# Performance work log

Measured on AMD Instinct MI355X. Metric: run time of the kernel, lower is better.

The kernel has to match this reference:

```python
import jax, jax.numpy as jnp
import numpy as np

N_NODES = 50000
N_EDGES = 800000
IN_FEAT = 128
H_FEAT = 64
NUM_HEADS = 4
NEG_SLOPE = 0.2  # DGL GATConv default LeakyReLU slope


def _gat_conv(feat, src, dst, W, attn_l, attn_r, bias, num_heads, out_feats):
    # feat: [N, Din]; W: [Din, H*F]; attn_l/attn_r: [H, F]; bias: [H*F]
    N = feat.shape[0]
    h = (feat @ W).reshape(N, num_heads, out_feats)          # [N, H, F]
    el = jnp.sum(h * attn_l, axis=-1)                        # [N, H]
    er = jnp.sum(h * attn_r, axis=-1)                        # [N, H]
    e = jax.nn.leaky_relu(el[src] + er[dst], NEG_SLOPE)      # [E, H]
    # segment softmax over incoming edges of each destination node
    m = jax.ops.segment_max(e, dst, num_segments=N)          # [N, H]
    ex = jnp.exp(e - m[dst])                                 # [E, H]
    s = jax.ops.segment_sum(ex, dst, num_segments=N)         # [N, H]
    alpha = ex / s[dst]                                      # [E, H]
    # attn_drop omitted (eval-mode deterministic reference)
    msg = h[src] * alpha[:, :, None]                         # [E, H, F]
    out = jax.ops.segment_sum(msg, dst, num_segments=N)      # [N, H, F]
    return out + bias.reshape(1, num_heads, out_feats)


def setup_inputs() -> dict:
    key = jax.random.key(0)
    ks = jax.random.split(key, 16)
    feat = jax.random.normal(ks[0], (N_NODES, IN_FEAT), dtype=jnp.float32)
    src = jax.random.randint(ks[1], (N_EDGES,), 0, N_NODES)
    dst = jax.random.randint(ks[2], (N_EDGES,), 0, N_NODES)
    sc = 0.1
    H, F = NUM_HEADS, H_FEAT
    params = {
        'W1': jax.random.normal(ks[3], (IN_FEAT, H * F), dtype=jnp.float32) * sc,
        'al1': jax.random.normal(ks[4], (H, F), dtype=jnp.float32) * sc,
        'ar1': jax.random.normal(ks[5], (H, F), dtype=jnp.float32) * sc,
        'b1': jnp.zeros((H * F,), dtype=jnp.float32),
        'W2': jax.random.normal(ks[6], (H * F, H * F), dtype=jnp.float32) * sc,
        'al2': jax.random.normal(ks[7], (H, F), dtype=jnp.float32) * sc,
        'ar2': jax.random.normal(ks[8], (H, F), dtype=jnp.float32) * sc,
        'b2': jnp.zeros((H * F,), dtype=jnp.float32),
        'W3': jax.random.normal(ks[9], (H * F, F), dtype=jnp.float32) * sc,
        'al3': jax.random.normal(ks[10], (1, F), dtype=jnp.float32) * sc,
        'ar3': jax.random.normal(ks[11], (1, F), dtype=jnp.float32) * sc,
        'b3': jnp.zeros((F,), dtype=jnp.float32),
    }
    return {'feat': feat, 'src': src, 'dst': dst, **params}


def reference(feat, src, dst, W1, al1, ar1, b1, W2, al2, ar2, b2, W3, al3, ar3, b3):
    h = _gat_conv(feat, src, dst, W1, al1, ar1, b1, NUM_HEADS, H_FEAT)
    h = jax.nn.relu(h.reshape(h.shape[0], -1))               # flatten(1) + relu
    h = _gat_conv(h, src, dst, W2, al2, ar2, b2, NUM_HEADS, H_FEAT)
    h = jax.nn.relu(h.reshape(h.shape[0], -1))
    h = _gat_conv(h, src, dst, W3, al3, ar3, b3, 1, H_FEAT)
    return h.mean(axis=1)                                    # [N, h_feat]
```

## Files before the change

### kernel.cpp

```cpp
#include <hip/hip_runtime.h>
#include <math.h>

#define N_NODES 50000
#define N_EDGES 800000

typedef short bf8 __attribute__((ext_vector_type(8)));
typedef float f4x __attribute__((ext_vector_type(4)));
typedef float f2v __attribute__((ext_vector_type(2)));
typedef unsigned short us8 __attribute__((ext_vector_type(8)));

__device__ __forceinline__ unsigned short f2bf(float x) {
  unsigned u = __float_as_uint(x);
  unsigned r = (u + 0x7fff + ((u >> 16) & 1)) >> 16;
  return (unsigned short)r;
}
__device__ __forceinline__ float bf2f(unsigned short b) {
  return __uint_as_float(((unsigned)b) << 16);
}
__device__ __forceinline__ unsigned pack2(float lo, float hi) {
  return (unsigned)f2bf(lo) | ((unsigned)f2bf(hi) << 16);
}
__device__ __forceinline__ f2v bfpair(unsigned d) {
  f2v r;
  r.x = __uint_as_float(d << 16);
  r.y = __uint_as_float(d & 0xffff0000u);
  return r;
}

template <int ABF16>
__global__ __launch_bounds__(256) void gemm_mfma_k(
    const void* __restrict__ Xv, const float* __restrict__ W,
    unsigned short* __restrict__ Yb, float* __restrict__ el,
    float* __restrict__ er, const float* __restrict__ al,
    const float* __restrict__ ar, int N, int K, int M) {
  __shared__ unsigned short As[128][40];
  __shared__ unsigned short Bs[64][40];
  const int tile_n = blockIdx.x * 128;
  const int cb = blockIdx.y * 64;
  const int t = threadIdx.x;
  const int wave = t >> 6, lane = t & 63;
  const int quad = lane >> 4, l16 = lane & 15;

  f4x acc[2][4];
#pragma unroll
  for (int i = 0; i < 2; ++i)
#pragma unroll
    for (int j = 0; j < 4; ++j) acc[i][j] = (f4x){0.f, 0.f, 0.f, 0.f};

  const int ar_ = t >> 1;
  const int ac0 = (t & 1) * 16;
  const int bn = t & 63;
  const int bkq = t >> 6;

  for (int k0 = 0; k0 < K; k0 += 32) {
    if (ABF16) {
      const unsigned short* Xb = (const unsigned short*)Xv;
      int gr = tile_n + ar_;
      us8 u0 = (us8)0, u1 = (us8)0;
      if (gr < N) {
        const unsigned short* s = Xb + (size_t)gr * K + k0 + ac0;
        u0 = *(const us8*)(s + 0);
        u1 = *(const us8*)(s + 8);
      }
      *(us8*)&As[ar_][ac0] = u0;
      *(us8*)&As[ar_][ac0 + 8] = u1;
    } else {
      const float* X = (const float*)Xv;
      int gr = tile_n + ar_;
      uint4 u0, u1;
      if (gr < N) {
        const float* s = X + (size_t)gr * K + k0 + ac0;
        float4 a = *(const float4*)(s + 0);
        float4 b = *(const float4*)(s + 4);
        float4 c = *(const float4*)(s + 8);
        float4 d = *(const float4*)(s + 12);
        u0 = make_uint4(pack2(a.x, a.y), pack2(a.z, a.w),
                        pack2(b.x, b.y), pack2(b.z, b.w));
        u1 = make_uint4(pack2(c.x, c.y), pack2(c.z, c.w),
                        pack2(d.x, d.y), pack2(d.z, d.w));
      } else {
        u0 = make_uint4(0, 0, 0, 0);
        u1 = make_uint4(0, 0, 0, 0);
      }
      *(uint4*)&As[ar_][ac0] = u0;
      *(uint4*)&As[ar_][ac0 + 8] = u1;
    }
    {
      const float* s = W + (size_t)(k0 + bkq * 8) * M + cb + bn;
      float w0 = s[0 * M], w1 = s[1 * M], w2 = s[2 * M], w3 = s[3 * M];
      float w4 = s[4 * M], w5 = s[5 * M], w6 = s[6 * M], w7 = s[7 * M];
      uint4 u = make_uint4(pack2(w0, w1), pack2(w2, w3), pack2(w4, w5),
                           pack2(w6, w7));
      *(uint4*)&Bs[bn][bkq * 8] = u;
    }
    __syncthreads();
    bf8 afrag[2], bfrag[4];
#pragma unroll
    for (int rt = 0; rt < 2; ++rt)
      afrag[rt] = *(const bf8*)&As[wave * 32 + rt * 16 + l16][quad * 8];
#pragma unroll
    for (int ct = 0; ct < 4; ++ct)
      bfrag[ct] = *(const bf8*)&Bs[ct * 16 + l16][quad * 8];
#pragma unroll
    for (int rt = 0; rt < 2; ++rt)
#pragma unroll
      for (int ct = 0; ct < 4; ++ct)
        acc[rt][ct] = __builtin_amdgcn_mfma_f32_16x16x32_bf16(
            afrag[rt], bfrag[ct], acc[rt][ct], 0, 0, 0);
    __syncthreads();
  }
  const int H = M >> 6;
  const int head = cb >> 6;
  float al4[4], ar4[4];
#pragma unroll
  for (int ct = 0; ct < 4; ++ct) {
    al4[ct] = al[cb + ct * 16 + l16];
    ar4[ct] = ar[cb + ct * 16 + l16];
  }
#pragma unroll
  for (int rt = 0; rt < 2; ++rt) {
#pragma unroll
    for (int r = 0; r < 4; ++r) {
      int row = tile_n + wave * 32 + rt * 16 + quad * 4 + r;
      float pl = 0.f, pr = 0.f;
#pragma unroll
      for (int ct = 0; ct < 4; ++ct) {
        float y = acc[rt][ct][r];
        pl += y * al4[ct];
        pr += y * ar4[ct];
        if (row < N) Yb[(size_t)row * M + cb + ct * 16 + l16] = f2bf(y);
      }
#pragma unroll
      for (int off = 1; off < 16; off <<= 1) {
        pl += __shfl_xor(pl, off);
        pr += __shfl_xor(pr, off);
      }
      if (l16 == 0 && row < N) {
        el[row * H + head] = pl;
        er[row * H + head] = pr;
      }
    }
  }
}

__global__ __launch_bounds__(256) void count_deg_k(
    const int* __restrict__ dst, int* __restrict__ deg, int E) {
  int e = blockIdx.x * blockDim.x + threadIdx.x;
  if (e < E) atomicAdd(&deg[dst[e]], 1);
}

__global__ __launch_bounds__(256) void alloc_rows_k(
    const int* __restrict__ deg, int* __restrict__ rowstart,
    int* __restrict__ cursor, int* __restrict__ gcounter, int N) {
  int i = blockIdx.x * blockDim.x + threadIdx.x;
  int lane = threadIdx.x & 63;
  int d = (i < N) ? deg[i] : 0;
  int x = d;
#pragma unroll
  for (int off = 1; off < 64; off <<= 1) {
    int t = __shfl_up(x, off);
    if (lane >= off) x += t;
  }
  int wsum = __shfl(x, 63);
  int base = 0;
  if (lane == 63) base = atomicAdd(gcounter, wsum);
  base = __shfl(base, 63);
  if (i < N) {
    int mystart = base + x - d;
    rowstart[i] = mystart;
    cursor[i] = mystart;
  }
}

__global__ __launch_bounds__(256) void scatter_k(
    const int* __restrict__ src, const int* __restrict__ dst,
    int* __restrict__ cursor, int* __restrict__ src_sorted, int E) {
  int e = blockIdx.x * blockDim.x + threadIdx.x;
  if (e < E) {
    int p = atomicAdd(&cursor[dst[e]], 1);
    src_sorted[p] = src[e];
  }
}

template <int RELU>
__global__ __launch_bounds__(256) void node_agg4_k(
    const unsigned short* __restrict__ hb, const float* __restrict__ el,
    const float* __restrict__ er, const int* __restrict__ rowstart,
    const int* __restrict__ rowend, const int* __restrict__ src_sorted,
    float* __restrict__ albuf, const float* __restrict__ bias,
    unsigned short* __restrict__ outb, int N) {
  int node = blockIdx.x * 4 + (threadIdx.x >> 6);
  int lane = threadIdx.x & 63;
  if (node >= N) return;
  int start = rowstart[node], end = rowend[node];
  int head1 = lane & 3;
  int slot = lane >> 2;
  float er_v = er[node * 4 + head1];
  float ssum = 0.f;
  for (int p = start + slot; p < end; p += 16) {
    int s = src_sorted[p];
    float v = el[s * 4 + head1] + er_v;
    v = (v >= 0.f) ? v : 0.2f * v;
    float ex = __expf(v);
    ssum += ex;
    albuf[p * 4 + head1] = ex;
  }
#pragma unroll
  for (int off = 4; off < 64; off <<= 1) ssum += __shfl_xor(ssum, off);
  float inv_s = (end > start) ? 1.f / ssum : 0.f;
  int eslot = lane >> 5;
  int flane = lane & 31;
  int fo8 = flane << 3;
  int headf = fo8 >> 6;
  float inv_f = __shfl(inv_s, headf);
  __builtin_amdgcn_s_waitcnt(0);
  f2v acc2[4];
#pragma unroll
  for (int q = 0; q < 4; ++q) acc2[q] = (f2v){0.f, 0.f};
  if (end > start) {
    int src_first = src_sorted[start];
    for (int p0 = start; p0 < end; p0 += 16) {
      int sj[8];
      float aj[8];
#pragma unroll
      for (int j = 0; j < 8; ++j) {
        int p = p0 + 2 * j + eslot;
        bool v = p < end;
        sj[j] = v ? src_sorted[p] : src_first;
        aj[j] = v ? albuf[p * 4 + headf] : 0.f;
      }
#pragma unroll
      for (int j = 0; j < 8; ++j) {
        uint4 d = *(const uint4*)(hb + (size_t)sj[j] * 256 + fo8);
        f2v a2 = (f2v){aj[j], aj[j]};
        acc2[0] += bfpair(d.x) * a2;
        acc2[1] += bfpair(d.y) * a2;
        acc2[2] += bfpair(d.z) * a2;
        acc2[3] += bfpair(d.w) * a2;
      }
    }
  }
  float acc[8];
#pragma unroll
  for (int q = 0; q < 4; ++q) {
    acc[2 * q] = acc2[q].x;
    acc[2 * q + 1] = acc2[q].y;
  }
#pragma unroll
  for (int q = 0; q < 8; ++q) acc[q] += __shfl_xor(acc[q], 32);
  if (eslot == 0) {
    us8 o;
#pragma unroll
    for (int q = 0; q < 8; ++q) {
      float v = acc[q] * inv_f + bias[fo8 + q];
      if (RELU) v = fmaxf(v, 0.f);
      o[q] = f2bf(v);
    }
    *(us8*)(outb + (size_t)node * 256 + fo8) = o;
  }
}

__global__ __launch_bounds__(256) void node_agg1_k(
    const unsigned short* __restrict__ hb, const float* __restrict__ el,
    const float* __restrict__ er, const int* __restrict__ rowstart,
    const int* __restrict__ rowend, const int* __restrict__ src_sorted,
    float* __restrict__ albuf, const float* __restrict__ bias,
    float* __restrict__ out, int N) {
  int node = blockIdx.x * 4 + (threadIdx.x >> 6);
  int lane = threadIdx.x & 63;
  if (node >= N) return;
  int start = rowstart[node], end = rowend[node];
  float er_v = er[node];
  float ssum = 0.f;
  for (int p = start + lane; p < end; p += 64) {
    float v = el[src_sorted[p]] + er_v;
    v = (v >= 0.f) ? v : 0.2f * v;
    float ex = __expf(v);
    ssum += ex;
    albuf[p] = ex;
  }
#pragma unroll
  for (int off = 1; off < 64; off <<= 1) ssum += __shfl_xor(ssum, off);
  float inv_s = (end > start) ? 1.f / ssum : 0.f;
  int eslot = lane >> 3;
  int flane = lane & 7;
  int fo8 = flane << 3;
  __builtin_amdgcn_s_waitcnt(0);
  f2v acc2[4];
#pragma unroll
  for (int q = 0; q < 4; ++q) acc2[q] = (f2v){0.f, 0.f};
  if (end > start) {
    int src_first = src_sorted[start];
    for (int p0 = start; p0 < end; p0 += 32) {
      int sj[4];
      float aj[4];
#pragma unroll
      for (int j = 0; j < 4; ++j) {
        int p = p0 + 8 * j + eslot;
        bool v = p < end;
        sj[j] = v ? src_sorted[p] : src_first;
        aj[j] = v ? albuf[p] : 0.f;
      }
#pragma unroll
      for (int j = 0; j < 4; ++j) {
        uint4 d = *(const uint4*)(hb + (size_t)sj[j] * 64 + fo8);
        f2v a2 = (f2v){aj[j], aj[j]};
        acc2[0] += bfpair(d.x) * a2;
        acc2[1] += bfpair(d.y) * a2;
        acc2[2] += bfpair(d.z) * a2;
        acc2[3] += bfpair(d.w) * a2;
      }
    }
  }
  float acc[8];
#pragma unroll
  for (int q = 0; q < 4; ++q) {
    acc[2 * q] = acc2[q].x;
    acc[2 * q + 1] = acc2[q].y;
  }
#pragma unroll
  for (int off = 8; off < 64; off <<= 1)
#pragma unroll
    for (int q = 0; q < 8; ++q) acc[q] += __shfl_xor(acc[q], off);
  if (eslot == 0) {
    float* o = out + (size_t)node * 64 + fo8;
#pragma unroll
    for (int q = 0; q < 8; ++q) o[q] = acc[q] * inv_s + bias[fo8 + q];
  }
}

extern "C" void kernel_launch(void* const* d_in, const int* in_sizes, int n_in,
                              void* d_out, int out_size, void* d_ws,
                              size_t ws_size, hipStream_t stream) {
  const float* feat = (const float*)d_in[0];
  const int* src = (const int*)d_in[1];
  const int* dst = (const int*)d_in[2];
  const float* W1 = (const float*)d_in[3];
  const float* al1 = (const float*)d_in[4];
  const float* ar1 = (const float*)d_in[5];
  const float* b1 = (const float*)d_in[6];
  const float* W2 = (const float*)d_in[7];
  const float* al2 = (const float*)d_in[8];
  const float* ar2 = (const float*)d_in[9];
  const float* b2 = (const float*)d_in[10];
  const float* W3 = (const float*)d_in[11];
  const float* al3 = (const float*)d_in[12];
  const float* ar3 = (const float*)d_in[13];
  const float* b3 = (const float*)d_in[14];
  float* out = (float*)d_out;

  unsigned short* hb = (unsigned short*)d_ws;
  unsigned short* fb = hb + (size_t)N_NODES * 256;
  float* el = (float*)(fb + (size_t)N_NODES * 256);
  float* er = el + (size_t)N_NODES * 4;
  int* rowstart = (int*)(er + (size_t)N_NODES * 4);
  int* cursor = rowstart + N_NODES;
  int* deg = cursor + N_NODES;
  int* gcounter = deg + N_NODES;
  int* src_sorted = gcounter + 1;
  float* albuf = (float*)(src_sorted + N_EDGES);

  const int N = N_NODES, E = N_EDGES;
  const int GX = (N + 127) / 128;

  hipMemsetAsync(deg, 0, (size_t)(N + 1) * sizeof(int), stream);
  hipLaunchKernelGGL(count_deg_k, dim3((E + 255) / 256), dim3(256), 0, stream,
                     dst, deg, E);
  hipLaunchKernelGGL(alloc_rows_k, dim3((N + 255) / 256), dim3(256), 0, stream,
                     deg, rowstart, cursor, gcounter, N);
  hipLaunchKernelGGL(scatter_k, dim3((E + 255) / 256), dim3(256), 0, stream,
                     src, dst, cursor, src_sorted, E);

  hipLaunchKernelGGL((gemm_mfma_k<0>), dim3(GX, 4), dim3(256), 0, stream, feat,
                     W1, hb, el, er, al1, ar1, N, 128, 256);
  hipLaunchKernelGGL((node_agg4_k<1>), dim3((N + 3) / 4), dim3(256), 0, stream,
                     hb, el, er, rowstart, cursor, src_sorted, albuf, b1, fb,
                     N);

  hipLaunchKernelGGL((gemm_mfma_k<1>), dim3(GX, 4), dim3(256), 0, stream, fb,
                     W2, hb, el, er, al2, ar2, N, 256, 256);
  hipLaunchKernelGGL((node_agg4_k<1>), dim3((N + 3) / 4), dim3(256), 0, stream,
                     hb, el, er, rowstart, cursor, src_sorted, albuf, b2, fb,
                     N);

  hipLaunchKernelGGL((gemm_mfma_k<1>), dim3(GX, 1), dim3(256), 0, stream, fb,
                     W3, hb, el, er, al3, ar3, N, 256, 64);
  hipLaunchKernelGGL(node_agg1_k, dim3((N + 3) / 4), dim3(256), 0, stream, hb,
                     el, er, rowstart, cursor, src_sorted, albuf, b3, out, N);
}
```

Before: 425.7 us.

## Double-buffer GEMM LDS tiles, vectorize CSR build, shrink aggregation edge batches

The GEMM now keeps two LDS buffers and prefetches the next K tile into registers while MFMAs run on the current one, which removes one barrier per iteration. Degree counting and scatter each handle two edges per thread through int2 loads. The aggregation kernels process half as many edges per loop iteration, which lowers register pressure but exposes less memory-level parallelism per wave.

```diff
diff --git a/kernel.cpp b/kernel.cpp
--- a/kernel.cpp
+++ b/kernel.cpp
@@ -33,8 +33,8 @@
     unsigned short* __restrict__ Yb, float* __restrict__ el,
     float* __restrict__ er, const float* __restrict__ al,
     const float* __restrict__ ar, int N, int K, int M) {
-  __shared__ unsigned short As[128][40];
-  __shared__ unsigned short Bs[64][40];
+  __shared__ unsigned short As[2][128][40];
+  __shared__ unsigned short Bs[2][64][40];
   const int tile_n = blockIdx.x * 128;
   const int cb = blockIdx.y * 64;
   const int t = threadIdx.x;
@@ -51,63 +51,66 @@
   const int ac0 = (t & 1) * 16;
   const int bn = t & 63;
   const int bkq = t >> 6;
-
-  for (int k0 = 0; k0 < K; k0 += 32) {
+  const int gr = tile_n + ar_;
+
+  uint4 a_u0, a_u1, b_u;
+  auto load_tile = [&](int k0) {
     if (ABF16) {
       const unsigned short* Xb = (const unsigned short*)Xv;
-      int gr = tile_n + ar_;
       us8 u0 = (us8)0, u1 = (us8)0;
       if (gr < N) {
         const unsigned short* s = Xb + (size_t)gr * K + k0 + ac0;
         u0 = *(const us8*)(s + 0);
         u1 = *(const us8*)(s + 8);
       }
-      *(us8*)&As[ar_][ac0] = u0;
-      *(us8*)&As[ar_][ac0 + 8] = u1;
+      a_u0 = *(const uint4*)&u0;
+      a_u1 = *(const uint4*)&u1;
     } else {
       const float* X = (const float*)Xv;
-      int gr = tile_n + ar_;
-      uint4 u0, u1;
       if (gr < N) {
         const float* s = X + (size_t)gr * K + k0 + ac0;
         float4 a = *(const float4*)(s + 0);
         float4 b = *(const float4*)(s + 4);
         float4 c = *(const float4*)(s + 8);
         float4 d = *(const float4*)(s + 12);
-        u0 = make_uint4(pack2(a.x, a.y), pack2(a.z, a.w),
-                        pack2(b.x, b.y), pack2(b.z, b.w));
-        u1 = make_uint4(pack2(c.x, c.y), pack2(c.z, c.w),
-                        pack2(d.x, d.y), pack2(d.z, d.w));
+        a_u0 = make_uint4(pack2(a.x, a.y), pack2(a.z, a.w),
+                          pack2(b.x, b.y), pack2(b.z, b.w));
+        a_u1 = make_uint4(pack2(c.x, c.y), pack2(c.z, c.w),
+                          pack2(d.x, d.y), pack2(d.z, d.w));
       } else {
-        u0 = make_uint4(0, 0, 0, 0);
-        u1 = make_uint4(0, 0, 0, 0);
-      }
-      *(uint4*)&As[ar_][ac0] = u0;
-      *(uint4*)&As[ar_][ac0 + 8] = u1;
+        a_u0 = make_uint4(0, 0, 0, 0);
+        a_u1 = make_uint4(0, 0, 0, 0);
+      }
     }
-    {
-      const float* s = W + (size_t)(k0 + bkq * 8) * M + cb + bn;
-      float w0 = s[0 * M], w1 = s[1 * M], w2 = s[2 * M], w3 = s[3 * M];
-      float w4 = s[4 * M], w5 = s[5 * M], w6 = s[6 * M], w7 = s[7 * M];
-      uint4 u = make_uint4(pack2(w0, w1), pack2(w2, w3), pack2(w4, w5),
-                           pack2(w6, w7));
-      *(uint4*)&Bs[bn][bkq * 8] = u;
-    }
+    const float* s = W + (size_t)(k0 + bkq * 8) * M + cb + bn;
+    float w0 = s[0 * M], w1 = s[1 * M], w2 = s[2 * M], w3 = s[3 * M];
+    float w4 = s[4 * M], w5 = s[5 * M], w6 = s[6 * M], w7 = s[7 * M];
+    b_u = make_uint4(pack2(w0, w1), pack2(w2, w3), pack2(w4, w5),
+                     pack2(w6, w7));
+  };
+
+  load_tile(0);
+  int cur = 0;
+  for (int k0 = 0; k0 < K; k0 += 32) {
+    *(uint4*)&As[cur][ar_][ac0] = a_u0;
+    *(uint4*)&As[cur][ar_][ac0 + 8] = a_u1;
+    *(uint4*)&Bs[cur][bn][bkq * 8] = b_u;
     __syncthreads();
+    if (k0 + 32 < K) load_tile(k0 + 32);
     bf8 afrag[2], bfrag[4];
 #pragma unroll
     for (int rt = 0; rt < 2; ++rt)
-      afrag[rt] = *(const bf8*)&As[wave * 32 + rt * 16 + l16][quad * 8];
+      afrag[rt] = *(const bf8*)&As[cur][wave * 32 + rt * 16 + l16][quad * 8];
 #pragma unroll
     for (int ct = 0; ct < 4; ++ct)
-      bfrag[ct] = *(const bf8*)&Bs[ct * 16 + l16][quad * 8];
+      bfrag[ct] = *(const bf8*)&Bs[cur][ct * 16 + l16][quad * 8];
 #pragma unroll
     for (int rt = 0; rt < 2; ++rt)
 #pragma unroll
       for (int ct = 0; ct < 4; ++ct)
         acc[rt][ct] = __builtin_amdgcn_mfma_f32_16x16x32_bf16(
             afrag[rt], bfrag[ct], acc[rt][ct], 0, 0, 0);
-    __syncthreads();
+    cur ^= 1;
   }
   const int H = M >> 6;
   const int head = cb >> 6;
@@ -144,9 +147,13 @@
 }
 
 __global__ __launch_bounds__(256) void count_deg_k(
-    const int* __restrict__ dst, int* __restrict__ deg, int E) {
-  int e = blockIdx.x * blockDim.x + threadIdx.x;
-  if (e < E) atomicAdd(&deg[dst[e]], 1);
+    const int2* __restrict__ dst2, int* __restrict__ deg, int E2) {
+  int i = blockIdx.x * blockDim.x + threadIdx.x;
+  if (i < E2) {
+    int2 d = dst2[i];
+    atomicAdd(&deg[d.x], 1);
+    atomicAdd(&deg[d.y], 1);
+  }
 }
 
 __global__ __launch_bounds__(256) void alloc_rows_k(
@@ -173,12 +180,16 @@
 }
 
 __global__ __launch_bounds__(256) void scatter_k(
-    const int* __restrict__ src, const int* __restrict__ dst,
-    int* __restrict__ cursor, int* __restrict__ src_sorted, int E) {
-  int e = blockIdx.x * blockDim.x + threadIdx.x;
-  if (e < E) {
-    int p = atomicAdd(&cursor[dst[e]], 1);
-    src_sorted[p] = src[e];
+    const int2* __restrict__ src2, const int2* __restrict__ dst2,
+    int* __restrict__ cursor, int* __restrict__ src_sorted, int E2) {
+  int i = blockIdx.x * blockDim.x + threadIdx.x;
+  if (i < E2) {
+    int2 s = src2[i];
+    int2 d = dst2[i];
+    int p0 = atomicAdd(&cursor[d.x], 1);
+    src_sorted[p0] = s.x;
+    int p1 = atomicAdd(&cursor[d.y], 1);
+    src_sorted[p1] = s.y;
   }
 }
 
@@ -219,18 +230,18 @@
   for (int q = 0; q < 4; ++q) acc2[q] = (f2v){0.f, 0.f};
   if (end > start) {
     int src_first = src_sorted[start];
-    for (int p0 = start; p0 < end; p0 += 16) {
-      int sj[8];
-      float aj[8];
-#pragma unroll
-      for (int j = 0; j < 8; ++j) {
+    for (int p0 = start; p0 < end; p0 += 8) {
+      int sj[4];
+      float aj[4];
+#pragma unroll
+      for (int j = 0; j < 4; ++j) {
         int p = p0 + 2 * j + eslot;
         bool v = p < end;
         sj[j] = v ? src_sorted[p] : src_first;
         aj[j] = v ? albuf[p * 4 + headf] : 0.f;
       }
 #pragma unroll
-      for (int j = 0; j < 8; ++j) {
+      for (int j = 0; j < 4; ++j) {
         uint4 d = *(const uint4*)(hb + (size_t)sj[j] * 256 + fo8);
         f2v a2 = (f2v){aj[j], aj[j]};
         acc2[0] += bfpair(d.x) * a2;
@@ -291,18 +302,18 @@
   for (int q = 0; q < 4; ++q) acc2[q] = (f2v){0.f, 0.f};
   if (end > start) {
     int src_first = src_sorted[start];
-    for (int p0 = start; p0 < end; p0 += 32) {
-      int sj[4];
-      float aj[4];
-#pragma unroll
-      for (int j = 0; j < 4; ++j) {
+    for (int p0 = start; p0 < end; p0 += 16) {
+      int sj[2];
+      float aj[2];
+#pragma unroll
+      for (int j = 0; j < 2; ++j) {
         int p = p0 + 8 * j + eslot;
         bool v = p < end;
         sj[j] = v ? src_sorted[p] : src_first;
         aj[j] = v ? albuf[p] : 0.f;
       }
 #pragma unroll
-      for (int j = 0; j < 4; ++j) {
+      for (int j = 0; j < 2; ++j) {
         uint4 d = *(const uint4*)(hb + (size_t)sj[j] * 64 + fo8);
         f2v a2 = (f2v){aj[j], aj[j]};
         acc2[0] += bfpair(d.x) * a2;
@@ -361,15 +372,17 @@
   float* albuf = (float*)(src_sorted + N_EDGES);
 
   const int N = N_NODES, E = N_EDGES;
+  const int E2 = E / 2;
   const int GX = (N + 127) / 128;
 
   hipMemsetAsync(deg, 0, (size_t)(N + 1) * sizeof(int), stream);
-  hipLaunchKernelGGL(count_deg_k, dim3((E + 255) / 256), dim3(256), 0, stream,
-                     dst, deg, E);
+  hipLaunchKernelGGL(count_deg_k, dim3((E2 + 255) / 256), dim3(256), 0, stream,
+                     (const int2*)dst, deg, E2);
   hipLaunchKernelGGL(alloc_rows_k, dim3((N + 255) / 256), dim3(256), 0, stream,
                      deg, rowstart, cursor, gcounter, N);
-  hipLaunchKernelGGL(scatter_k, dim3((E + 255) / 256), dim3(256), 0, stream,
-                     src, dst, cursor, src_sorted, E);
+  hipLaunchKernelGGL(scatter_k, dim3((E2 + 255) / 256), dim3(256), 0, stream,
+                     (const int2*)src, (const int2*)dst, cursor, src_sorted,
+                     E2);
 
   hipLaunchKernelGGL((gemm_mfma_k<0>), dim3(GX, 4), dim3(256), 0, stream, feat,
                      W1, hb, el, er, al1, ar1, N, 128, 256);
```

New measurement: 437.6 us. 2.8% more time.
